# Performance work log

Measured on AMD Instinct MI355X. Metric: run time of the kernel, lower is better.

## Reference

```python
import jax, jax.numpy as jnp
import numpy as np

B, N, E, H, HEADS = 4, 10000, 160000, 128, 4
NEG_SLOPE = 0.2  # PyG GATConv default
LN_EPS = 1e-5


def setup_inputs() -> dict:
    key = jax.random.key(0)
    ks = jax.random.split(key, 24)
    inp = {}
    inp["node_embeddings"] = jax.random.normal(ks[0], (B, N, H), dtype=jnp.float32)
    inp["src_index"] = jax.random.randint(ks[1], (B, E), 0, N)
    inp["tgt_index"] = jax.random.randint(ks[2], (B, E), 0, N)
    sc = 1.0 / np.sqrt(H)
    for i in range(3):
        j = 3 + 3 * i
        inp[f"W{i+1}"] = jax.random.normal(ks[j], (H, HEADS * H), dtype=jnp.float32) * sc
        inp[f"att_src{i+1}"] = jax.random.normal(ks[j + 1], (HEADS, H), dtype=jnp.float32) * sc
        inp[f"att_dst{i+1}"] = jax.random.normal(ks[j + 2], (HEADS, H), dtype=jnp.float32) * sc
        inp[f"bias{i+1}"] = jnp.zeros((H,), dtype=jnp.float32)
    inp["ln1_g"] = jnp.ones((H,), dtype=jnp.float32)
    inp["ln1_b"] = jnp.zeros((H,), dtype=jnp.float32)
    inp["ln2_g"] = jnp.ones((H,), dtype=jnp.float32)
    inp["ln2_b"] = jnp.zeros((H,), dtype=jnp.float32)
    return inp


def _layer_norm(x, g, b):
    mu = jnp.mean(x, axis=-1, keepdims=True)
    var = jnp.mean((x - mu) ** 2, axis=-1, keepdims=True)
    return (x - mu) * jax.lax.rsqrt(var + LN_EPS) * g + b


def _gat(x, src, tgt, W, a_s, a_d, b):
    # x: [N, H]; src/tgt: [E'] (self-loops already appended). eval mode -> no dropout.
    h = (x @ W).reshape(N, HEADS, H)               # [N, heads, H]
    e_src = jnp.einsum('nhc,hc->nh', h, a_s)       # [N, heads]
    e_dst = jnp.einsum('nhc,hc->nh', h, a_d)
    e = jax.nn.leaky_relu(e_src[src] + e_dst[tgt], NEG_SLOPE)  # [E', heads]
    m = jax.ops.segment_max(e, tgt, num_segments=N)            # per-target max
    ex = jnp.exp(e - m[tgt])
    s = jax.ops.segment_sum(ex, tgt, num_segments=N)
    alpha = ex / s[tgt]                                        # [E', heads]
    out = jax.ops.segment_sum(alpha[:, :, None] * h[src], tgt, num_segments=N)
    return out.mean(axis=1) + b                                # concat=False -> head mean


def reference(node_embeddings, src_index, tgt_index,
              W1, att_src1, att_dst1, bias1,
              W2, att_src2, att_dst2, bias2,
              W3, att_src3, att_dst3, bias3,
              ln1_g, ln1_b, ln2_g, ln2_b):
    loop = jnp.arange(N, dtype=src_index.dtype)

    def one_graph(x, src, tgt):
        s = jnp.concatenate([src, loop])   # GATConv add_self_loops=True (default)
        t = jnp.concatenate([tgt, loop])
        m = _gat(x, s, t, W1, att_src1, att_dst1, bias1)
        m = jax.nn.relu(_layer_norm(m, ln1_g, ln1_b))
        m = _gat(m, s, t, W2, att_src2, att_dst2, bias2)
        m = jax.nn.relu(_layer_norm(m, ln2_g, ln2_b))
        m = _gat(m, s, t, W3, att_src3, att_dst3, bias3)
        return m

    return jax.vmap(one_graph)(node_embeddings, src_index, tgt_index)
```

## Files before the change

kernel.cpp:

```cpp
#include <hip/hip_runtime.h>
#include <hip/hip_bf16.h>
#include <cstdint>
#include <cstddef>

#define B_ 4
#define N_ 10000
#define E_ 160000
#define H_ 128
#define HEADS_ 4
#define HH_ 512
#define NROWS (B_*N_)

typedef __attribute__((ext_vector_type(8))) short bf16x8;
typedef __attribute__((ext_vector_type(4))) float f32x4;
typedef __attribute__((ext_vector_type(2))) float f32x2;

__device__ __forceinline__ float lrelu(float x){ return x > 0.f ? x : 0.2f*x; }
__device__ __forceinline__ unsigned short f2b(float f){
  unsigned int u = __builtin_bit_cast(unsigned int, f);
  unsigned int r = (u + 0x7fffu + ((u >> 16) & 1u)) >> 16;
  return (unsigned short)r;
}
__device__ __forceinline__ float blo(unsigned int u){ return __builtin_bit_cast(float, u << 16); }
__device__ __forceinline__ float bhi(unsigned int u){ return __builtin_bit_cast(float, u & 0xffff0000u); }

__global__ void k_count(const int* __restrict__ tgt, int* __restrict__ cnt){
  int e = blockIdx.x*blockDim.x + threadIdx.x;
  int b = blockIdx.y;
  int t = tgt[(size_t)b*E_ + e];
  atomicAdd(&cnt[b*N_ + t], 1);
}

__global__ void k_scan(const int* __restrict__ cnt, int* __restrict__ off, int* __restrict__ cursor){
  int b = blockIdx.x;
  __shared__ int wsum[16];
  __shared__ int carry_s;
  int lane = threadIdx.x & 63, wid = threadIdx.x >> 6;
  if (threadIdx.x == 0){ carry_s = 0; off[b*(N_+1)] = 0; }
  __syncthreads();
  for (int base = 0; base < N_; base += 1024){
    int i = base + threadIdx.x;
    int v = (i < N_) ? cnt[b*N_ + i] : 0;
    int x = v;
    #pragma unroll
    for (int d = 1; d < 64; d <<= 1){
      int y = __shfl_up(x, d);
      if (lane >= d) x += y;
    }
    if (lane == 63) wsum[wid] = x;
    __syncthreads();
    if (wid == 0 && lane < 16){
      int w = wsum[lane];
      #pragma unroll
      for (int d = 1; d < 16; d <<= 1){
        int y = __shfl_up(w, d, 16);
        if (lane >= d) w += y;
      }
      wsum[lane] = w;
    }
    __syncthreads();
    int excl = (wid ? wsum[wid-1] : 0) + carry_s;
    if (i < N_){
      int inc = x + excl;
      off[b*(N_+1) + i + 1] = inc;
      cursor[b*N_ + i] = inc - v;
    }
    __syncthreads();
    if (threadIdx.x == 0) carry_s += wsum[15];
    __syncthreads();
  }
}

__global__ void k_scatter(const int* __restrict__ src, const int* __restrict__ tgt,
                          int* __restrict__ cursor, int* __restrict__ csr){
  int e = blockIdx.x*blockDim.x + threadIdx.x;
  int b = blockIdx.y;
  int t = tgt[(size_t)b*E_ + e];
  int pos = atomicAdd(&cursor[b*N_ + t], 1);
  csr[(size_t)b*E_ + pos] = src[(size_t)b*E_ + e];
}

__global__ void k_prep(const float* __restrict__ W0, const float* __restrict__ W1, const float* __restrict__ W2,
                       const float* __restrict__ as0, const float* __restrict__ as1, const float* __restrict__ as2,
                       const float* __restrict__ ad0, const float* __restrict__ ad1, const float* __restrict__ ad2,
                       float* __restrict__ wasA, float* __restrict__ wadA, unsigned short* __restrict__ wtA){
  int l = blockIdx.y;
  const float* W   = (l==0)?W0:(l==1)?W1:W2;
  const float* asp = (l==0)?as0:(l==1)?as1:as2;
  const float* adp = (l==0)?ad0:(l==1)?ad1:ad2;
  if (blockIdx.x < 256){
    int i = blockIdx.x*256 + threadIdx.x;
    int c = i >> 7, k = i & 127;
    wtA[(size_t)l*HH_*H_ + i] = f2b(W[(size_t)k*HH_ + c]);
  } else {
    int j = (blockIdx.x - 256)*256 + threadIdx.x;
    if (j < H_*HEADS_){
      int k = j >> 2, h = j & 3;
      const float* wrow = W + (size_t)k*HH_ + h*H_;
      const float* asr = asp + h*H_;
      const float* adr = adp + h*H_;
      float ss = 0.f, sd = 0.f;
      for (int c = 0; c < H_; ++c){ float w = wrow[c]; ss += w*asr[c]; sd += w*adr[c]; }
      wasA[l*HH_ + j] = ss; wadA[l*HH_ + j] = sd;
    }
  }
}

__global__ __launch_bounds__(256) void k_cast_logits(const float* __restrict__ X,
    const float* __restrict__ was, const float* __restrict__ wad,
    unsigned short* __restrict__ Xb, float* __restrict__ es, float* __restrict__ ed){
  int gw = (blockIdx.x*blockDim.x + threadIdx.x) >> 6;
  int lane = threadIdx.x & 63;
  float2 v = *(const float2*)(X + (size_t)gw*H_ + lane*2);
  unsigned int o = ((unsigned int)f2b(v.y) << 16) | (unsigned int)f2b(v.x);
  *(unsigned int*)(Xb + (size_t)gw*H_ + lane*2) = o;
  int c = lane*2;
  const f32x4* w4 = (const f32x4*)was;
  const f32x4* d4 = (const f32x4*)wad;
  f32x4 se = v.x*w4[c] + v.y*w4[c+1];
  f32x4 de = v.x*d4[c] + v.y*d4[c+1];
  #pragma unroll
  for (int d = 1; d < 64; d <<= 1){
    se.x += __shfl_xor(se.x,d); se.y += __shfl_xor(se.y,d);
    se.z += __shfl_xor(se.z,d); se.w += __shfl_xor(se.w,d);
    de.x += __shfl_xor(de.x,d); de.y += __shfl_xor(de.y,d);
    de.z += __shfl_xor(de.z,d); de.w += __shfl_xor(de.w,d);
  }
  if (lane == 0){
    *(float4*)(es + (size_t)gw*4) = make_float4(se.x, se.y, se.z, se.w);
    *(float4*)(ed + (size_t)gw*4) = make_float4(de.x, de.y, de.z, de.w);
  }
}

__global__ __launch_bounds__(256) void k_gemm_mfma(const unsigned short* __restrict__ Xb,
    const unsigned short* __restrict__ Wt, unsigned short* __restrict__ Hb){
  __shared__ unsigned short xs[64*128];
  __shared__ unsigned short ws[64*128];
  int row0 = blockIdx.x * 64, col0 = blockIdx.y * 64;
  int tid = threadIdx.x;
  int ch = tid & 15, r0 = tid >> 4;
  #pragma unroll
  for (int p = 0; p < 4; ++p){
    int r = r0 + p*16;
    int sc = ch ^ (r & 7);
    *(uint4*)(&xs[r*128 + sc*8]) = *(const uint4*)(Xb + (size_t)(row0 + r)*H_ + ch*8);
    *(uint4*)(&ws[r*128 + sc*8]) = *(const uint4*)(Wt + (size_t)(col0 + r)*H_ + ch*8);
  }
  __syncthreads();
  int w = tid >> 6, l = tid & 63;
  int lr = l & 15, q = l >> 4;
  f32x4 z = {0.f, 0.f, 0.f, 0.f};
  f32x4 acc[4] = {z, z, z, z};
  int arow = w*16 + lr;
  #pragma unroll
  for (int kf = 0; kf < 4; ++kf){
    int bch = kf*4 + q;
    bf16x8 a = *(const bf16x8*)(&xs[arow*128 + (bch ^ (arow & 7))*8]);
    #pragma unroll
    for (int cf = 0; cf < 4; ++cf){
      int brow = cf*16 + lr;
      bf16x8 bfr = *(const bf16x8*)(&ws[brow*128 + (bch ^ (brow & 7))*8]);
      acc[cf] = __builtin_amdgcn_mfma_f32_16x16x32_bf16(a, bfr, acc[cf], 0, 0, 0);
    }
  }
  #pragma unroll
  for (int cf = 0; cf < 4; ++cf){
    #pragma unroll
    for (int rg = 0; rg < 4; ++rg){
      int row = row0 + w*16 + q*4 + rg;
      int col = col0 + cf*16 + lr;
      Hb[(size_t)row*HH_ + col] = f2b(acc[cf][rg]);
    }
  }
}

template<bool FINAL>
__global__ __launch_bounds__(256) void k_aggregate(
    const unsigned short* __restrict__ Hb,
    const float* __restrict__ es, const float* __restrict__ ed,
    const int* __restrict__ off, const int* __restrict__ csr,
    const float* __restrict__ bias,
    const float* __restrict__ wasN, const float* __restrict__ wadN,
    const float* __restrict__ lng, const float* __restrict__ lnb,
    float* __restrict__ Yout, unsigned short* __restrict__ Xbout,
    float* __restrict__ esN, float* __restrict__ edN)
{
  __shared__ float alpha_s[4][64][4];
  __shared__ int   srcn_s[4][64];
  __shared__ float orow_s[4][128];
  int wv = threadIdx.x >> 6, lane = threadIdx.x & 63;
  int gw = blockIdx.x*4 + wv;
  int b = gw / N_, t = gw - b*N_;
  const float4 edv = *(const float4*)(ed + (size_t)gw*4);
  int start = off[b*(N_+1) + t];
  int deg = off[b*(N_+1) + t + 1] - start;
  int total = deg + 1;
  const int* lst = csr + (size_t)b*E_ + start;
  const float* esb = es + (size_t)b*N_*4;
  int head = lane >> 4;
  int cb = head*H_ + (lane & 15)*8;
  const unsigned short* hbase = Hb + (size_t)b*N_*HH_;
  f32x2 zz = {0.f, 0.f};
  f32x2 ac[4] = {zz, zz, zz, zz};

  if (total <= 64){
    bool valid = lane < total;
    int srcn = (lane < deg) ? lst[lane] : t;
    srcn_s[wv][lane] = srcn;
    float4 ev = *(const float4*)(esb + (size_t)srcn*4);
    float e0 = valid ? lrelu(ev.x + edv.x) : -1e30f;
    float e1 = valid ? lrelu(ev.y + edv.y) : -1e30f;
    float e2 = valid ? lrelu(ev.z + edv.z) : -1e30f;
    float e3 = valid ? lrelu(ev.w + edv.w) : -1e30f;
    float M0 = e0, M1 = e1, M2 = e2, M3 = e3;
    #pragma unroll
    for (int d = 1; d < 64; d <<= 1){
      M0 = fmaxf(M0, __shfl_xor(M0, d)); M1 = fmaxf(M1, __shfl_xor(M1, d));
      M2 = fmaxf(M2, __shfl_xor(M2, d)); M3 = fmaxf(M3, __shfl_xor(M3, d));
    }
    float p0 = valid ? __expf(e0 - M0) : 0.f;
    float p1 = valid ? __expf(e1 - M1) : 0.f;
    float p2 = valid ? __expf(e2 - M2) : 0.f;
    float p3 = valid ? __expf(e3 - M3) : 0.f;
    float S0 = p0, S1 = p1, S2 = p2, S3 = p3;
    #pragma unroll
    for (int d = 1; d < 64; d <<= 1){
      S0 += __shfl_xor(S0, d); S1 += __shfl_xor(S1, d);
      S2 += __shfl_xor(S2, d); S3 += __shfl_xor(S3, d);
    }
    *(float4*)(&alpha_s[wv][lane][0]) = make_float4(p0/S0, p1/S1, p2/S2, p3/S3);
    __builtin_amdgcn_wave_barrier();

    int i = 0;
    for (; i + 2 <= total; i += 2){
      int sA = srcn_s[wv][i];
      int sB = srcn_s[wv][i+1];
      float aA = alpha_s[wv][i][head];
      float aB = alpha_s[wv][i+1][head];
      uint4 hA = *(const uint4*)(hbase + (size_t)sA*HH_ + cb);
      uint4 hB = *(const uint4*)(hbase + (size_t)sB*HH_ + cb);
      f32x2 vA = {aA, aA}, vB = {aB, aB};
      ac[0] += vA * (f32x2){blo(hA.x), bhi(hA.x)};
      ac[1] += vA * (f32x2){blo(hA.y), bhi(hA.y)};
      ac[2] += vA * (f32x2){blo(hA.z), bhi(hA.z)};
      ac[3] += vA * (f32x2){blo(hA.w), bhi(hA.w)};
      ac[0] += vB * (f32x2){blo(hB.x), bhi(hB.x)};
      ac[1] += vB * (f32x2){blo(hB.y), bhi(hB.y)};
      ac[2] += vB * (f32x2){blo(hB.z), bhi(hB.z)};
      ac[3] += vB * (f32x2){blo(hB.w), bhi(hB.w)};
    }
    if (i < total){
      int sA = srcn_s[wv][i];
      float aA = alpha_s[wv][i][head];
      uint4 hA = *(const uint4*)(hbase + (size_t)sA*HH_ + cb);
      f32x2 vA = {aA, aA};
      ac[0] += vA * (f32x2){blo(hA.x), bhi(hA.x)};
      ac[1] += vA * (f32x2){blo(hA.y), bhi(hA.y)};
      ac[2] += vA * (f32x2){blo(hA.z), bhi(hA.z)};
      ac[3] += vA * (f32x2){blo(hA.w), bhi(hA.w)};
    }
  } else {
    float m0=-1e30f, m1=-1e30f, m2=-1e30f, m3=-1e30f;
    float s0=0.f, s1=0.f, s2=0.f, s3=0.f;
    for (int i2 = lane; i2 <= deg; i2 += 64){
      int srcn = (i2 < deg) ? lst[i2] : t;
      float4 ev = *(const float4*)(esb + (size_t)srcn*4);
      float e0 = lrelu(ev.x + edv.x);
      float e1 = lrelu(ev.y + edv.y);
      float e2 = lrelu(ev.z + edv.z);
      float e3 = lrelu(ev.w + edv.w);
      float nm;
      nm = fmaxf(m0, e0); s0 = s0*__expf(m0-nm) + __expf(e0-nm); m0 = nm;
      nm = fmaxf(m1, e1); s1 = s1*__expf(m1-nm) + __expf(e1-nm); m1 = nm;
      nm = fmaxf(m2, e2); s2 = s2*__expf(m2-nm) + __expf(e2-nm); m2 = nm;
      nm = fmaxf(m3, e3); s3 = s3*__expf(m3-nm) + __expf(e3-nm); m3 = nm;
    }
    #pragma unroll
    for (int d = 1; d < 64; d <<= 1){
      float om, os, nm;
      om = __shfl_xor(m0, d); os = __shfl_xor(s0, d); nm = fmaxf(m0, om);
      s0 = s0*__expf(m0-nm) + os*__expf(om-nm); m0 = nm;
      om = __shfl_xor(m1, d); os = __shfl_xor(s1, d); nm = fmaxf(m1, om);
      s1 = s1*__expf(m1-nm) + os*__expf(om-nm); m1 = nm;
      om = __shfl_xor(m2, d); os = __shfl_xor(s2, d); nm = fmaxf(m2, om);
      s2 = s2*__expf(m2-nm) + os*__expf(om-nm); m2 = nm;
      om = __shfl_xor(m3, d); os = __shfl_xor(s3, d); nm = fmaxf(m3, om);
      s3 = s3*__expf(m3-nm) + os*__expf(om-nm); m3 = nm;
    }
    float mh, sh, edh;
    if      (head == 0){ mh = m0; sh = s0; edh = edv.x; }
    else if (head == 1){ mh = m1; sh = s1; edh = edv.y; }
    else if (head == 2){ mh = m2; sh = s2; edh = edv.z; }
    else               { mh = m3; sh = s3; edh = edv.w; }
    float rh = 1.0f / sh;
    for (int i2 = 0; i2 < total; ++i2){
      int srcn = (i2 < deg) ? lst[i2] : t;
      float eh = esb[(size_t)srcn*4 + head];
      float al = __expf(lrelu(eh + edh) - mh) * rh;
      uint4 hA = *(const uint4*)(hbase + (size_t)srcn*HH_ + cb);
      f32x2 vA = {al, al};
      ac[0] += vA * (f32x2){blo(hA.x), bhi(hA.x)};
      ac[1] += vA * (f32x2){blo(hA.y), bhi(hA.y)};
      ac[2] += vA * (f32x2){blo(hA.z), bhi(hA.z)};
      ac[3] += vA * (f32x2){blo(hA.w), bhi(hA.w)};
    }
  }

  float a[8] = {ac[0].x, ac[0].y, ac[1].x, ac[1].y, ac[2].x, ac[2].y, ac[3].x, ac[3].y};
  #pragma unroll
  for (int d = 16; d < 64; d <<= 1)
    #pragma unroll
    for (int j = 0; j < 8; j++) a[j] += __shfl_xor(a[j], d);

  int c = (lane & 15)*8;
  if (FINAL){
    if (lane < 16){
      float4 o0 = make_float4(0.25f*a[0]+bias[c+0], 0.25f*a[1]+bias[c+1],
                              0.25f*a[2]+bias[c+2], 0.25f*a[3]+bias[c+3]);
      float4 o1 = make_float4(0.25f*a[4]+bias[c+4], 0.25f*a[5]+bias[c+5],
                              0.25f*a[6]+bias[c+6], 0.25f*a[7]+bias[c+7]);
      *(float4*)(Yout + (size_t)gw*H_ + c)     = o0;
      *(float4*)(Yout + (size_t)gw*H_ + c + 4) = o1;
    }
  } else {
    float o[8];
    #pragma unroll
    for (int j = 0; j < 8; j++) o[j] = 0.25f*a[j] + bias[c+j];
    float ss = 0.f;
    #pragma unroll
    for (int j = 0; j < 8; j++) ss += o[j];
    #pragma unroll
    for (int d = 1; d < 16; d <<= 1) ss += __shfl_xor(ss, d);
    float mu = ss * (1.f/H_);
    float vv = 0.f;
    #pragma unroll
    for (int j = 0; j < 8; j++){ float dx = o[j]-mu; vv += dx*dx; }
    #pragma unroll
    for (int d = 1; d < 16; d <<= 1) vv += __shfl_xor(vv, d);
    float inv = rsqrtf(vv*(1.f/H_) + 1e-5f);
    float4 g0 = *(const float4*)(lng + c), g1 = *(const float4*)(lng + c + 4);
    float4 b0 = *(const float4*)(lnb + c), b1 = *(const float4*)(lnb + c + 4);
    float gg[8] = {g0.x,g0.y,g0.z,g0.w,g1.x,g1.y,g1.z,g1.w};
    float bb[8] = {b0.x,b0.y,b0.z,b0.w,b1.x,b1.y,b1.z,b1.w};
    float oo[8];
    #pragma unroll
    for (int j = 0; j < 8; j++) oo[j] = fmaxf((o[j]-mu)*inv*gg[j] + bb[j], 0.f);
    if (lane < 16){
      uint4 up;
      up.x = ((unsigned int)f2b(oo[1]) << 16) | f2b(oo[0]);
      up.y = ((unsigned int)f2b(oo[3]) << 16) | f2b(oo[2]);
      up.z = ((unsigned int)f2b(oo[5]) << 16) | f2b(oo[4]);
      up.w = ((unsigned int)f2b(oo[7]) << 16) | f2b(oo[6]);
      *(uint4*)(Xbout + (size_t)gw*H_ + lane*8) = up;
      *(float4*)(&orow_s[wv][c])     = make_float4(oo[0], oo[1], oo[2], oo[3]);
      *(float4*)(&orow_s[wv][c + 4]) = make_float4(oo[4], oo[5], oo[6], oo[7]);
    }
    __builtin_amdgcn_wave_barrier();
    float pe = 0.f, pd = 0.f;
    #pragma unroll
    for (int j = 0; j < 8; j++){
      float xv = orow_s[wv][c + j];
      pe += xv * wasN[(c + j)*4 + head];
      pd += xv * wadN[(c + j)*4 + head];
    }
    #pragma unroll
    for (int d = 1; d < 16; d <<= 1){ pe += __shfl_xor(pe, d); pd += __shfl_xor(pd, d); }
    if ((lane & 15) == 0){
      esN[(size_t)gw*4 + head] = pe;
      edN[(size_t)gw*4 + head] = pd;
    }
  }
}

extern "C" void kernel_launch(void* const* d_in, const int* in_sizes, int n_in,
                              void* d_out, int out_size, void* d_ws, size_t ws_size,
                              hipStream_t stream){
  const float* x0   = (const float*)d_in[0];
  const int*   srcI = (const int*)d_in[1];
  const int*   tgtI = (const int*)d_in[2];
  const float* Wl[3]  = {(const float*)d_in[3], (const float*)d_in[7],  (const float*)d_in[11]};
  const float* asl[3] = {(const float*)d_in[4], (const float*)d_in[8],  (const float*)d_in[12]};
  const float* adl[3] = {(const float*)d_in[5], (const float*)d_in[9],  (const float*)d_in[13]};
  const float* bl[3]  = {(const float*)d_in[6], (const float*)d_in[10], (const float*)d_in[14]};
  const float* lng[2] = {(const float*)d_in[15], (const float*)d_in[17]};
  const float* lnb[2] = {(const float*)d_in[16], (const float*)d_in[18]};

  char* p = (char*)d_ws;
  auto carve = [&](size_t bytes) -> void* {
    void* r = (void*)p; p += (bytes + 255) & ~(size_t)255; return r;
  };
  int*   off    = (int*)carve((size_t)B_*(N_+1)*4);
  int*   cnt    = (int*)carve((size_t)B_*N_*4);
  int*   cursor = (int*)carve((size_t)B_*N_*4);
  int*   csr    = (int*)carve((size_t)B_*E_*4);
  float* es2[2] = {(float*)carve((size_t)NROWS*4*4), (float*)carve((size_t)NROWS*4*4)};
  float* ed2[2] = {(float*)carve((size_t)NROWS*4*4), (float*)carve((size_t)NROWS*4*4)};
  float* wasA   = (float*)carve((size_t)3*HH_*4);
  float* wadA   = (float*)carve((size_t)3*HH_*4);
  unsigned short* wtA  = (unsigned short*)carve((size_t)3*HH_*H_*2);
  unsigned short* hbuf = (unsigned short*)carve((size_t)NROWS*HH_*2);
  unsigned short* xbf  = (unsigned short*)carve((size_t)NROWS*H_*2);

  hipMemsetAsync(cnt, 0, (size_t)B_*N_*4, stream);
  k_count  <<<dim3(E_/256, B_), 256, 0, stream>>>(tgtI, cnt);
  k_scan   <<<B_, 1024, 0, stream>>>(cnt, off, cursor);
  k_scatter<<<dim3(E_/256, B_), 256, 0, stream>>>(srcI, tgtI, cursor, csr);
  k_prep   <<<dim3(258, 3), 256, 0, stream>>>(Wl[0], Wl[1], Wl[2],
                                              asl[0], asl[1], asl[2],
                                              adl[0], adl[1], adl[2],
                                              wasA, wadA, wtA);
  k_cast_logits<<<NROWS/4, 256, 0, stream>>>(x0, wasA, wadA, xbf, es2[0], ed2[0]);

  for (int l = 0; l < 3; ++l){
    k_gemm_mfma<<<dim3(NROWS/64, HH_/64), 256, 0, stream>>>(xbf, wtA + (size_t)l*HH_*H_, hbuf);
    int cur = l & 1, nxt = cur ^ 1;
    if (l < 2){
      k_aggregate<false><<<NROWS/4, 256, 0, stream>>>(hbuf, es2[cur], ed2[cur], off, csr, bl[l],
          wasA + (size_t)(l+1)*HH_, wadA + (size_t)(l+1)*HH_, lng[l], lnb[l],
          nullptr, xbf, es2[nxt], ed2[nxt]);
    } else {
      k_aggregate<true><<<NROWS/4, 256, 0, stream>>>(hbuf, es2[cur], ed2[cur], off, csr, bl[l],
          nullptr, nullptr, nullptr, nullptr,
          (float*)d_out, nullptr, nullptr, nullptr);
    }
  }
}
```

Measured before the change: 488.6 us.

## Software-pipeline neighbor gathers four rows at a time in GAT aggregation

The small-degree aggregation path now gathers neighbor feature rows in groups of four and double-buffers them, so the next group's loads are issued while the current group is accumulated. The goal is more memory-level parallelism and hidden gather latency. The alpha shared buffer is transposed to a head-major layout with padding, so the four per-head weights and source indices can each be fetched with one vector load. In exchange, the loop reads padded slots up to a multiple of four and holds more registers live for the eight in-flight rows, which may cut occupancy.

```diff
diff --git a/kernel.cpp b/kernel.cpp
--- a/kernel.cpp
+++ b/kernel.cpp
@@ -23,6 +23,14 @@
 }
 __device__ __forceinline__ float blo(unsigned int u){ return __builtin_bit_cast(float, u << 16); }
 __device__ __forceinline__ float bhi(unsigned int u){ return __builtin_bit_cast(float, u & 0xffff0000u); }
+
+__device__ __forceinline__ void acc_row(f32x2* ac, float al, uint4 h){
+  f32x2 v = {al, al};
+  ac[0] += v * (f32x2){blo(h.x), bhi(h.x)};
+  ac[1] += v * (f32x2){blo(h.y), bhi(h.y)};
+  ac[2] += v * (f32x2){blo(h.z), bhi(h.z)};
+  ac[3] += v * (f32x2){blo(h.w), bhi(h.w)};
+}
 
 __global__ void k_count(const int* __restrict__ tgt, int* __restrict__ cnt){
   int e = blockIdx.x*blockDim.x + threadIdx.x;
@@ -185,7 +193,7 @@
     float* __restrict__ Yout, unsigned short* __restrict__ Xbout,
     float* __restrict__ esN, float* __restrict__ edN)
 {
-  __shared__ float alpha_s[4][64][4];
+  __shared__ float alpha_s[4][4][68];
   __shared__ int   srcn_s[4][64];
   __shared__ float orow_s[4][128];
   int wv = threadIdx.x >> 6, lane = threadIdx.x & 63;
@@ -228,36 +236,51 @@
       S0 += __shfl_xor(S0, d); S1 += __shfl_xor(S1, d);
       S2 += __shfl_xor(S2, d); S3 += __shfl_xor(S3, d);
     }
-    *(float4*)(&alpha_s[wv][lane][0]) = make_float4(p0/S0, p1/S1, p2/S2, p3/S3);
+    alpha_s[wv][0][lane] = p0/S0;
+    alpha_s[wv][1][lane] = p1/S1;
+    alpha_s[wv][2][lane] = p2/S2;
+    alpha_s[wv][3][lane] = p3/S3;
     __builtin_amdgcn_wave_barrier();
 
-    int i = 0;
-    for (; i + 2 <= total; i += 2){
-      int sA = srcn_s[wv][i];
-      int sB = srcn_s[wv][i+1];
-      float aA = alpha_s[wv][i][head];
-      float aB = alpha_s[wv][i+1][head];
-      uint4 hA = *(const uint4*)(hbase + (size_t)sA*HH_ + cb);
-      uint4 hB = *(const uint4*)(hbase + (size_t)sB*HH_ + cb);
-      f32x2 vA = {aA, aA}, vB = {aB, aB};
-      ac[0] += vA * (f32x2){blo(hA.x), bhi(hA.x)};
-      ac[1] += vA * (f32x2){blo(hA.y), bhi(hA.y)};
-      ac[2] += vA * (f32x2){blo(hA.z), bhi(hA.z)};
-      ac[3] += vA * (f32x2){blo(hA.w), bhi(hA.w)};
-      ac[0] += vB * (f32x2){blo(hB.x), bhi(hB.x)};
-      ac[1] += vB * (f32x2){blo(hB.y), bhi(hB.y)};
-      ac[2] += vB * (f32x2){blo(hB.z), bhi(hB.z)};
-      ac[3] += vB * (f32x2){blo(hB.w), bhi(hB.w)};
-    }
-    if (i < total){
-      int sA = srcn_s[wv][i];
-      float aA = alpha_s[wv][i][head];
-      uint4 hA = *(const uint4*)(hbase + (size_t)sA*HH_ + cb);
-      f32x2 vA = {aA, aA};
-      ac[0] += vA * (f32x2){blo(hA.x), bhi(hA.x)};
-      ac[1] += vA * (f32x2){blo(hA.y), bhi(hA.y)};
-      ac[2] += vA * (f32x2){blo(hA.z), bhi(hA.z)};
-      ac[3] += vA * (f32x2){blo(hA.w), bhi(hA.w)};
+    const float* alp = &alpha_s[wv][head][0];
+    const int*   srp = &srcn_s[wv][0];
+    auto gat = [&](int s){ return *(const uint4*)(hbase + (size_t)s*HH_ + cb); };
+    int nIter = (total + 3) >> 2;
+    float4 alA, alB;
+    uint4 a0, a1, a2, a3, b0, b1, b2, b3;
+    {
+      alA = *(const float4*)(alp);
+      int4 s4 = *(const int4*)(srp);
+      a0 = gat(s4.x); a1 = gat(s4.y); a2 = gat(s4.z); a3 = gat(s4.w);
+    }
+    int it = 1;
+    while (true){
+      if (it == nIter){
+        acc_row(ac, alA.x, a0); acc_row(ac, alA.y, a1);
+        acc_row(ac, alA.z, a2); acc_row(ac, alA.w, a3);
+        break;
+      }
+      {
+        alB = *(const float4*)(alp + it*4);
+        int4 s4 = *(const int4*)(srp + it*4);
+        b0 = gat(s4.x); b1 = gat(s4.y); b2 = gat(s4.z); b3 = gat(s4.w);
+      }
+      acc_row(ac, alA.x, a0); acc_row(ac, alA.y, a1);
+      acc_row(ac, alA.z, a2); acc_row(ac, alA.w, a3);
+      ++it;
+      if (it == nIter){
+        acc_row(ac, alB.x, b0); acc_row(ac, alB.y, b1);
+        acc_row(ac, alB.z, b2); acc_row(ac, alB.w, b3);
+        break;
+      }
+      {
+        alA = *(const float4*)(alp + it*4);
+        int4 s4 = *(const int4*)(srp + it*4);
+        a0 = gat(s4.x); a1 = gat(s4.y); a2 = gat(s4.z); a3 = gat(s4.w);
+      }
+      acc_row(ac, alB.x, b0); acc_row(ac, alB.y, b1);
+      acc_row(ac, alB.z, b2); acc_row(ac, alB.w, b3);
+      ++it;
     }
   } else {
     float m0=-1e30f, m1=-1e30f, m2=-1e30f, m3=-1e30f;
@@ -298,11 +321,7 @@
       float eh = esb[(size_t)srcn*4 + head];
       float al = __expf(lrelu(eh + edh) - mh) * rh;
       uint4 hA = *(const uint4*)(hbase + (size_t)srcn*HH_ + cb);
-      f32x2 vA = {al, al};
-      ac[0] += vA * (f32x2){blo(hA.x), bhi(hA.x)};
-      ac[1] += vA * (f32x2){blo(hA.y), bhi(hA.y)};
-      ac[2] += vA * (f32x2){blo(hA.z), bhi(hA.z)};
-      ac[3] += vA * (f32x2){blo(hA.w), bhi(hA.w)};
+      acc_row(ac, al, hA);
     }
   }
 
```

New measurement: 487.1 us. About the same (-0.3%).

## Split each node's edge aggregation across two waves and recompute alpha inline

Applied to the files above, without the earlier changes.

The aggregate kernel now gives each target node two waves instead of one. Each wave gathers alternate pairs of edges, and the two partial sums are combined through shared memory after a block barrier before the bias, LayerNorm and next-layer logit epilogue. Attention weights are no longer staged in shared memory; each lane recomputes its head's alpha from the source logit and the wave-reduced max and sum. This doubles the number of in-flight gathers per node to hide memory latency. The cost is twice as many blocks, a __syncthreads, redundant softmax statistics computed by both waves, and an epilogue run by only half the waves.

```diff
diff --git a/kernel.cpp b/kernel.cpp
--- a/kernel.cpp
+++ b/kernel.cpp
@@ -23,6 +23,14 @@
 }
 __device__ __forceinline__ float blo(unsigned int u){ return __builtin_bit_cast(float, u << 16); }
 __device__ __forceinline__ float bhi(unsigned int u){ return __builtin_bit_cast(float, u & 0xffff0000u); }
+
+__device__ __forceinline__ void acc_row(f32x2* ac, float al, uint4 h){
+  f32x2 v = {al, al};
+  ac[0] += v * (f32x2){blo(h.x), bhi(h.x)};
+  ac[1] += v * (f32x2){blo(h.y), bhi(h.y)};
+  ac[2] += v * (f32x2){blo(h.z), bhi(h.z)};
+  ac[3] += v * (f32x2){blo(h.w), bhi(h.w)};
+}
 
 __global__ void k_count(const int* __restrict__ tgt, int* __restrict__ cnt){
   int e = blockIdx.x*blockDim.x + threadIdx.x;
@@ -185,11 +193,12 @@
     float* __restrict__ Yout, unsigned short* __restrict__ Xbout,
     float* __restrict__ esN, float* __restrict__ edN)
 {
-  __shared__ float alpha_s[4][64][4];
-  __shared__ int   srcn_s[4][64];
-  __shared__ float orow_s[4][128];
+  __shared__ float part_s[2][16][8];
+  __shared__ float orow_s[2][128];
   int wv = threadIdx.x >> 6, lane = threadIdx.x & 63;
-  int gw = blockIdx.x*4 + wv;
+  int nd = wv >> 1;
+  int pw = wv & 1;
+  int gw = blockIdx.x*2 + nd;
   int b = gw / N_, t = gw - b*N_;
   const float4 edv = *(const float4*)(ed + (size_t)gw*4);
   int start = off[b*(N_+1) + t];
@@ -200,13 +209,12 @@
   int head = lane >> 4;
   int cb = head*H_ + (lane & 15)*8;
   const unsigned short* hbase = Hb + (size_t)b*N_*HH_;
-  f32x2 zz = {0.f, 0.f};
-  f32x2 ac[4] = {zz, zz, zz, zz};
+  float edh = head==0 ? edv.x : head==1 ? edv.y : head==2 ? edv.z : edv.w;
+  float Mh, rSh;
 
   if (total <= 64){
     bool valid = lane < total;
     int srcn = (lane < deg) ? lst[lane] : t;
-    srcn_s[wv][lane] = srcn;
     float4 ev = *(const float4*)(esb + (size_t)srcn*4);
     float e0 = valid ? lrelu(ev.x + edv.x) : -1e30f;
     float e1 = valid ? lrelu(ev.y + edv.y) : -1e30f;
@@ -228,37 +236,9 @@
       S0 += __shfl_xor(S0, d); S1 += __shfl_xor(S1, d);
       S2 += __shfl_xor(S2, d); S3 += __shfl_xor(S3, d);
     }
-    *(float4*)(&alpha_s[wv][lane][0]) = make_float4(p0/S0, p1/S1, p2/S2, p3/S3);
-    __builtin_amdgcn_wave_barrier();
-
-    int i = 0;
-    for (; i + 2 <= total; i += 2){
-      int sA = srcn_s[wv][i];
-      int sB = srcn_s[wv][i+1];
-      float aA = alpha_s[wv][i][head];
-      float aB = alpha_s[wv][i+1][head];
-      uint4 hA = *(const uint4*)(hbase + (size_t)sA*HH_ + cb);
-      uint4 hB = *(const uint4*)(hbase + (size_t)sB*HH_ + cb);
-      f32x2 vA = {aA, aA}, vB = {aB, aB};
-      ac[0] += vA * (f32x2){blo(hA.x), bhi(hA.x)};
-      ac[1] += vA * (f32x2){blo(hA.y), bhi(hA.y)};
-      ac[2] += vA * (f32x2){blo(hA.z), bhi(hA.z)};
-      ac[3] += vA * (f32x2){blo(hA.w), bhi(hA.w)};
-      ac[0] += vB * (f32x2){blo(hB.x), bhi(hB.x)};
-      ac[1] += vB * (f32x2){blo(hB.y), bhi(hB.y)};
-      ac[2] += vB * (f32x2){blo(hB.z), bhi(hB.z)};
-      ac[3] += vB * (f32x2){blo(hB.w), bhi(hB.w)};
-    }
-    if (i < total){
-      int sA = srcn_s[wv][i];
-      float aA = alpha_s[wv][i][head];
-      uint4 hA = *(const uint4*)(hbase + (size_t)sA*HH_ + cb);
-      f32x2 vA = {aA, aA};
-      ac[0] += vA * (f32x2){blo(hA.x), bhi(hA.x)};
-      ac[1] += vA * (f32x2){blo(hA.y), bhi(hA.y)};
-      ac[2] += vA * (f32x2){blo(hA.z), bhi(hA.z)};
-      ac[3] += vA * (f32x2){blo(hA.w), bhi(hA.w)};
-    }
+    Mh = head==0 ? M0 : head==1 ? M1 : head==2 ? M2 : M3;
+    float Sh = head==0 ? S0 : head==1 ? S1 : head==2 ? S2 : S3;
+    rSh = 1.0f / Sh;
   } else {
     float m0=-1e30f, m1=-1e30f, m2=-1e30f, m3=-1e30f;
     float s0=0.f, s1=0.f, s2=0.f, s3=0.f;
@@ -287,23 +267,32 @@
       om = __shfl_xor(m3, d); os = __shfl_xor(s3, d); nm = fmaxf(m3, om);
       s3 = s3*__expf(m3-nm) + os*__expf(om-nm); m3 = nm;
     }
-    float mh, sh, edh;
-    if      (head == 0){ mh = m0; sh = s0; edh = edv.x; }
-    else if (head == 1){ mh = m1; sh = s1; edh = edv.y; }
-    else if (head == 2){ mh = m2; sh = s2; edh = edv.z; }
-    else               { mh = m3; sh = s3; edh = edv.w; }
-    float rh = 1.0f / sh;
-    for (int i2 = 0; i2 < total; ++i2){
-      int srcn = (i2 < deg) ? lst[i2] : t;
-      float eh = esb[(size_t)srcn*4 + head];
-      float al = __expf(lrelu(eh + edh) - mh) * rh;
-      uint4 hA = *(const uint4*)(hbase + (size_t)srcn*HH_ + cb);
-      f32x2 vA = {al, al};
-      ac[0] += vA * (f32x2){blo(hA.x), bhi(hA.x)};
-      ac[1] += vA * (f32x2){blo(hA.y), bhi(hA.y)};
-      ac[2] += vA * (f32x2){blo(hA.z), bhi(hA.z)};
-      ac[3] += vA * (f32x2){blo(hA.w), bhi(hA.w)};
-    }
+    Mh = head==0 ? m0 : head==1 ? m1 : head==2 ? m2 : m3;
+    float Sh = head==0 ? s0 : head==1 ? s1 : head==2 ? s2 : s3;
+    rSh = 1.0f / Sh;
+  }
+
+  f32x2 zz = {0.f, 0.f};
+  f32x2 ac[4] = {zz, zz, zz, zz};
+  int i = pw;
+  for (; i + 2 < total; i += 4){
+    int sA = lst[i];
+    int sB = (i + 2 < deg) ? lst[i+2] : t;
+    float eA = esb[(size_t)sA*4 + head];
+    float eB = esb[(size_t)sB*4 + head];
+    uint4 hA = *(const uint4*)(hbase + (size_t)sA*HH_ + cb);
+    uint4 hB = *(const uint4*)(hbase + (size_t)sB*HH_ + cb);
+    float aA = __expf(lrelu(eA + edh) - Mh) * rSh;
+    float aB = __expf(lrelu(eB + edh) - Mh) * rSh;
+    acc_row(ac, aA, hA);
+    acc_row(ac, aB, hB);
+  }
+  if (i < total){
+    int sA = (i < deg) ? lst[i] : t;
+    float eA = esb[(size_t)sA*4 + head];
+    uint4 hA = *(const uint4*)(hbase + (size_t)sA*HH_ + cb);
+    float aA = __expf(lrelu(eA + edh) - Mh) * rSh;
+    acc_row(ac, aA, hA);
   }
 
   float a[8] = {ac[0].x, ac[0].y, ac[1].x, ac[1].y, ac[2].x, ac[2].y, ac[3].x, ac[3].y};
@@ -312,62 +301,77 @@
     #pragma unroll
     for (int j = 0; j < 8; j++) a[j] += __shfl_xor(a[j], d);
 
+  if (pw == 1 && lane < 16){
+    #pragma unroll
+    for (int j = 0; j < 8; j++) part_s[nd][lane][j] = a[j];
+  }
+  __syncthreads();
+
   int c = (lane & 15)*8;
-  if (FINAL){
+  if (pw == 0){
+    float tot[8];
     if (lane < 16){
-      float4 o0 = make_float4(0.25f*a[0]+bias[c+0], 0.25f*a[1]+bias[c+1],
-                              0.25f*a[2]+bias[c+2], 0.25f*a[3]+bias[c+3]);
-      float4 o1 = make_float4(0.25f*a[4]+bias[c+4], 0.25f*a[5]+bias[c+5],
-                              0.25f*a[6]+bias[c+6], 0.25f*a[7]+bias[c+7]);
-      *(float4*)(Yout + (size_t)gw*H_ + c)     = o0;
-      *(float4*)(Yout + (size_t)gw*H_ + c + 4) = o1;
-    }
-  } else {
-    float o[8];
-    #pragma unroll
-    for (int j = 0; j < 8; j++) o[j] = 0.25f*a[j] + bias[c+j];
-    float ss = 0.f;
-    #pragma unroll
-    for (int j = 0; j < 8; j++) ss += o[j];
-    #pragma unroll
-    for (int d = 1; d < 16; d <<= 1) ss += __shfl_xor(ss, d);
-    float mu = ss * (1.f/H_);
-    float vv = 0.f;
-    #pragma unroll
-    for (int j = 0; j < 8; j++){ float dx = o[j]-mu; vv += dx*dx; }
-    #pragma unroll
-    for (int d = 1; d < 16; d <<= 1) vv += __shfl_xor(vv, d);
-    float inv = rsqrtf(vv*(1.f/H_) + 1e-5f);
-    float4 g0 = *(const float4*)(lng + c), g1 = *(const float4*)(lng + c + 4);
-    float4 b0 = *(const float4*)(lnb + c), b1 = *(const float4*)(lnb + c + 4);
-    float gg[8] = {g0.x,g0.y,g0.z,g0.w,g1.x,g1.y,g1.z,g1.w};
-    float bb[8] = {b0.x,b0.y,b0.z,b0.w,b1.x,b1.y,b1.z,b1.w};
-    float oo[8];
-    #pragma unroll
-    for (int j = 0; j < 8; j++) oo[j] = fmaxf((o[j]-mu)*inv*gg[j] + bb[j], 0.f);
-    if (lane < 16){
-      uint4 up;
-      up.x = ((unsigned int)f2b(oo[1]) << 16) | f2b(oo[0]);
-      up.y = ((unsigned int)f2b(oo[3]) << 16) | f2b(oo[2]);
-      up.z = ((unsigned int)f2b(oo[5]) << 16) | f2b(oo[4]);
-      up.w = ((unsigned int)f2b(oo[7]) << 16) | f2b(oo[6]);
-      *(uint4*)(Xbout + (size_t)gw*H_ + lane*8) = up;
-      *(float4*)(&orow_s[wv][c])     = make_float4(oo[0], oo[1], oo[2], oo[3]);
-      *(float4*)(&orow_s[wv][c + 4]) = make_float4(oo[4], oo[5], oo[6], oo[7]);
-    }
-    __builtin_amdgcn_wave_barrier();
-    float pe = 0.f, pd = 0.f;
-    #pragma unroll
-    for (int j = 0; j < 8; j++){
-      float xv = orow_s[wv][c + j];
-      pe += xv * wasN[(c + j)*4 + head];
-      pd += xv * wadN[(c + j)*4 + head];
-    }
-    #pragma unroll
-    for (int d = 1; d < 16; d <<= 1){ pe += __shfl_xor(pe, d); pd += __shfl_xor(pd, d); }
-    if ((lane & 15) == 0){
-      esN[(size_t)gw*4 + head] = pe;
-      edN[(size_t)gw*4 + head] = pd;
+      #pragma unroll
+      for (int j = 0; j < 8; j++) tot[j] = a[j] + part_s[nd][lane][j];
+    }
+    if (FINAL){
+      if (lane < 16){
+        float4 o0 = make_float4(0.25f*tot[0]+bias[c+0], 0.25f*tot[1]+bias[c+1],
+                                0.25f*tot[2]+bias[c+2], 0.25f*tot[3]+bias[c+3]);
+        float4 o1 = make_float4(0.25f*tot[4]+bias[c+4], 0.25f*tot[5]+bias[c+5],
+                                0.25f*tot[6]+bias[c+6], 0.25f*tot[7]+bias[c+7]);
+        *(float4*)(Yout + (size_t)gw*H_ + c)     = o0;
+        *(float4*)(Yout + (size_t)gw*H_ + c + 4) = o1;
+      }
+    } else {
+      float o[8];
+      float ss = 0.f;
+      if (lane < 16){
+        #pragma unroll
+        for (int j = 0; j < 8; j++){ o[j] = 0.25f*tot[j] + bias[c+j]; ss += o[j]; }
+      }
+      #pragma unroll
+      for (int d = 1; d < 16; d <<= 1) ss += __shfl_xor(ss, d);
+      float mu = ss * (1.f/H_);
+      float vv = 0.f;
+      if (lane < 16){
+        #pragma unroll
+        for (int j = 0; j < 8; j++){ float dx = o[j]-mu; vv += dx*dx; }
+      }
+      #pragma unroll
+      for (int d = 1; d < 16; d <<= 1) vv += __shfl_xor(vv, d);
+      float inv = rsqrtf(vv*(1.f/H_) + 1e-5f);
+      if (lane < 16){
+        float4 g0 = *(const float4*)(lng + c), g1 = *(const float4*)(lng + c + 4);
+        float4 b0 = *(const float4*)(lnb + c), b1 = *(const float4*)(lnb + c + 4);
+        float gg[8] = {g0.x,g0.y,g0.z,g0.w,g1.x,g1.y,g1.z,g1.w};
+        float bb[8] = {b0.x,b0.y,b0.z,b0.w,b1.x,b1.y,b1.z,b1.w};
+        float oo[8];
+        #pragma unroll
+        for (int j = 0; j < 8; j++) oo[j] = fmaxf((o[j]-mu)*inv*gg[j] + bb[j], 0.f);
+        uint4 up;
+        up.x = ((unsigned int)f2b(oo[1]) << 16) | f2b(oo[0]);
+        up.y = ((unsigned int)f2b(oo[3]) << 16) | f2b(oo[2]);
+        up.z = ((unsigned int)f2b(oo[5]) << 16) | f2b(oo[4]);
+        up.w = ((unsigned int)f2b(oo[7]) << 16) | f2b(oo[6]);
+        *(uint4*)(Xbout + (size_t)gw*H_ + lane*8) = up;
+        *(float4*)(&orow_s[nd][c])     = make_float4(oo[0], oo[1], oo[2], oo[3]);
+        *(float4*)(&orow_s[nd][c + 4]) = make_float4(oo[4], oo[5], oo[6], oo[7]);
+      }
+      __builtin_amdgcn_wave_barrier();
+      float pe = 0.f, pd = 0.f;
+      #pragma unroll
+      for (int j = 0; j < 8; j++){
+        float xv = orow_s[nd][c + j];
+        pe += xv * wasN[(c + j)*4 + head];
+        pd += xv * wadN[(c + j)*4 + head];
+      }
+      #pragma unroll
+      for (int d = 1; d < 16; d <<= 1){ pe += __shfl_xor(pe, d); pd += __shfl_xor(pd, d); }
+      if ((lane & 15) == 0){
+        esN[(size_t)gw*4 + head] = pe;
+        edN[(size_t)gw*4 + head] = pd;
+      }
     }
   }
 }
@@ -415,11 +419,11 @@
     k_gemm_mfma<<<dim3(NROWS/64, HH_/64), 256, 0, stream>>>(xbf, wtA + (size_t)l*HH_*H_, hbuf);
     int cur = l & 1, nxt = cur ^ 1;
     if (l < 2){
-      k_aggregate<false><<<NROWS/4, 256, 0, stream>>>(hbuf, es2[cur], ed2[cur], off, csr, bl[l],
+      k_aggregate<false><<<NROWS/2, 256, 0, stream>>>(hbuf, es2[cur], ed2[cur], off, csr, bl[l],
           wasA + (size_t)(l+1)*HH_, wadA + (size_t)(l+1)*HH_, lng[l], lnb[l],
           nullptr, xbf, es2[nxt], ed2[nxt]);
     } else {
-      k_aggregate<true><<<NROWS/4, 256, 0, stream>>>(hbuf, es2[cur], ed2[cur], off, csr, bl[l],
+      k_aggregate<true><<<NROWS/2, 256, 0, stream>>>(hbuf, es2[cur], ed2[cur], off, csr, bl[l],
           nullptr, nullptr, nullptr, nullptr,
           (float*)d_out, nullptr, nullptr, nullptr);
     }
```

After: 543.0 us. 1.11x slower.
